# Optimization experiments

Hardware: AMD Instinct MI355X
Metric: run time of the kernel (lower is better)

Reference implementation:

```python
import jax, jax.numpy as jnp
import numpy as np

H = 16  # num_attention_heads


def setup_inputs() -> dict:
    key = jax.random.key(0)
    ks = jax.random.split(key, 4)
    B, S, D = 2, 2048, 1024
    hidden_states = jax.random.normal(ks[0], (B, S, D), dtype=jnp.float32)
    attention_mask = jnp.zeros((B, 1, 1, S), dtype=jnp.float32)
    scale = 1.0 / np.sqrt(D)
    Wq = jax.random.normal(ks[1], (D, D), dtype=jnp.float32) * scale
    Wk = jax.random.normal(ks[2], (D, D), dtype=jnp.float32) * scale
    Wv = jax.random.normal(ks[3], (D, D), dtype=jnp.float32) * scale
    bq = jnp.zeros((D,), dtype=jnp.float32)
    bk = jnp.zeros((D,), dtype=jnp.float32)
    bv = jnp.zeros((D,), dtype=jnp.float32)
    return {"hidden_states": hidden_states, "attention_mask": attention_mask,
            "Wq": Wq, "bq": bq, "Wk": Wk, "bk": bk, "Wv": Wv, "bv": bv}


def reference(hidden_states, attention_mask, Wq, bq, Wk, bk, Wv, bv):
    B, S, D = hidden_states.shape
    Dh = D // H

    def proj(W, b):
        # torch Linear: x @ W.T + b ; reshape to [B, H, S, Dh]
        y = jnp.einsum('bsd,ed->bse', hidden_states, W) + b
        return y.reshape(B, S, H, Dh).transpose(0, 2, 1, 3)

    q = proj(Wq, bq)
    k = proj(Wk, bk)
    v = proj(Wv, bv)

    scores = jnp.einsum('bhqd,bhkd->bhqk', q, k) / jnp.sqrt(jnp.float32(Dh))
    scores = scores + attention_mask  # additive mask broadcast [B,1,1,S]
    probs = jax.nn.softmax(scores, axis=-1)  # [B,H,Sq,Sk]
    out_attention_scores = probs.sum(axis=-2).sum(axis=-2)  # [B, Sk]
    # dropout prob = 0 (eval) -> identity
    context = jnp.einsum('bhqk,bhkd->bhqd', probs, v)
    context = context.transpose(0, 2, 1, 3).reshape(B, S, D)
    return context, out_attention_scores
```

## Files before the change

### kernel.cpp

```cpp
#include <hip/hip_runtime.h>
#include <hip/hip_bf16.h>
#include <stdint.h>

typedef unsigned short u16;
typedef __attribute__((ext_vector_type(8))) unsigned short u16x8;
typedef __attribute__((ext_vector_type(4))) unsigned short u16x4;
typedef __attribute__((ext_vector_type(8))) __bf16 bf16x8;
typedef __attribute__((ext_vector_type(4))) float f32x4;
typedef __attribute__((ext_vector_type(16))) float f32x16;

#define LOG2E 1.44269504088896340736f

#if defined(__has_builtin)
#if __has_builtin(__builtin_amdgcn_exp2f)
#define EXP2(x) __builtin_amdgcn_exp2f(x)
#endif
#endif
#ifndef EXP2
#define EXP2(x) exp2f(x)
#endif

__device__ __forceinline__ f32x4 mfma16(u16x8 a, u16x8 b, f32x4 c) {
  return __builtin_amdgcn_mfma_f32_16x16x32_bf16(
      __builtin_bit_cast(bf16x8, a), __builtin_bit_cast(bf16x8, b), c, 0, 0, 0);
}

__device__ __forceinline__ f32x16 mfma32(u16x8 a, u16x8 b, f32x16 c) {
  return __builtin_amdgcn_mfma_f32_32x32x16_bf16(
      __builtin_bit_cast(bf16x8, a), __builtin_bit_cast(bf16x8, b), c, 0, 0, 0);
}

__device__ __forceinline__ u16 f2bf(float f) {
  unsigned u = __builtin_bit_cast(unsigned, f);
  return (u16)((u + 0x7fffu + ((u >> 16) & 1u)) >> 16);
}

__device__ __forceinline__ unsigned cvtpk(float a, float b) {
  unsigned r;
  asm volatile("v_cvt_pk_bf16_f32 %0, %1, %2" : "=v"(r) : "v"(a), "v"(b));
  return r;
}

__device__ __forceinline__ void pswap(unsigned& a, unsigned& b) {
  asm volatile("v_permlane32_swap_b32 %0, %1" : "+v"(a), "+v"(b));
}

__device__ __forceinline__ void gload_lds16(const void* g, void* l) {
  __builtin_amdgcn_global_load_lds(
      (__attribute__((address_space(1))) void*)const_cast<void*>(g),
      (__attribute__((address_space(3))) void*)l, 16, 0, 0);
}

template<int N> __device__ __forceinline__ void vmwait() {
  asm volatile("s_waitcnt vmcnt(%0)" :: "n"(N) : "memory");
  __builtin_amdgcn_sched_barrier(0);
}

#define SWZ(row, colbyte) ((((row) * 128) + (colbyte)) ^ (((row) & 7) << 4))

__global__ void cast_f32_bf16(const float* __restrict__ src, u16* __restrict__ dst, int n4) {
  int i = blockIdx.x * blockDim.x + threadIdx.x;
  if (i < n4) {
    f32x4 v = ((const f32x4*)src)[i];
    u16x4 o;
    o[0] = f2bf(v[0]); o[1] = f2bf(v[1]); o[2] = f2bf(v[2]); o[3] = f2bf(v[3]);
    ((u16x4*)dst)[i] = o;
  }
}

__global__ void cast3_f32_bf16(const float* __restrict__ s0, const float* __restrict__ s1,
                               const float* __restrict__ s2, u16* __restrict__ dst) {
  const int seg = blockIdx.x >> 10;
  const int i = (blockIdx.x & 1023) * blockDim.x + threadIdx.x;
  const float* src = (seg == 0) ? s0 : ((seg == 1) ? s1 : s2);
  f32x4 v = ((const f32x4*)src)[i];
  u16x4 o;
  o[0] = f2bf(v[0]); o[1] = f2bf(v[1]); o[2] = f2bf(v[2]); o[3] = f2bf(v[3]);
  ((u16x4*)(dst + (size_t)seg * 1048576))[i] = o;
}

__global__ __launch_bounds__(256) void gemm_qkv(
    const u16* __restrict__ A, const u16* __restrict__ Bm,
    const float* __restrict__ bq, const float* __restrict__ bk, const float* __restrict__ bv,
    u16* __restrict__ Qb, u16* __restrict__ Kb, u16* __restrict__ VTb) {
  __shared__ __align__(16) u16 Asm[3][4096];
  __shared__ __align__(16) u16 Bsm[3][4096];
  const int tid = threadIdx.x;
  const int wave = tid >> 6, lane = tid & 63;
  const int lq = lane & 15, lg = lane >> 4;
  const int wr = wave >> 1, wc = wave & 1;
  const int lin = blockIdx.y * 24 + blockIdx.x;
  const int wg = (lin & 7) * 96 + (lin >> 3);
  const int m0 = (wg / 24) * 128, n0 = (wg % 24) * 128;

  f32x4 zero = {0.f, 0.f, 0.f, 0.f};
  f32x4 acc[4][4];
#pragma unroll
  for (int mi = 0; mi < 4; ++mi)
#pragma unroll
    for (int ni = 0; ni < 4; ++ni) acc[mi][ni] = zero;

  auto stage = [&](int kt, int buf) {
    const int k0 = kt * 32;
#pragma unroll
    for (int c = 0; c < 2; ++c) {
      const int idx = wave * 2 + c;
      const u16* ga = A + (size_t)(m0 + idx * 16 + (lane >> 2)) * 1024 + k0 + (lane & 3) * 8;
      gload_lds16(ga, (char*)&Asm[buf][0] + idx * 1024);
      const u16* gb = Bm + (size_t)(n0 + idx * 16 + (lane >> 2)) * 1024 + k0 + (lane & 3) * 8;
      gload_lds16(gb, (char*)&Bsm[buf][0] + idx * 1024);
    }
  };

  stage(0, 0);
  stage(1, 1);
  for (int kt = 0; kt < 32; ++kt) {
    if (kt < 31) vmwait<4>(); else vmwait<0>();
    __builtin_amdgcn_s_barrier();
    if (kt + 2 < 32) stage(kt + 2, (kt + 2) % 3);
    const int cur = kt % 3;

    __builtin_amdgcn_s_setprio(1);
    u16x8 af[4], bfr[4];
#pragma unroll
    for (int mi = 0; mi < 4; ++mi)
      af[mi] = *(const u16x8*)&Asm[cur][(wr * 64 + mi * 16 + lq) * 32 + lg * 8];
#pragma unroll
    for (int ni = 0; ni < 4; ++ni)
      bfr[ni] = *(const u16x8*)&Bsm[cur][(wc * 64 + ni * 16 + lq) * 32 + lg * 8];
#pragma unroll
    for (int mi = 0; mi < 4; ++mi)
#pragma unroll
      for (int ni = 0; ni < 4; ++ni)
        acc[mi][ni] = mfma16(af[mi], bfr[ni], acc[mi][ni]);
    __builtin_amdgcn_s_setprio(0);
  }

  const int which = n0 >> 10;
  const float* bias = (which == 0) ? bq : ((which == 1) ? bk : bv);
  const float scl = (which == 0) ? (0.125f * LOG2E) : 1.0f;
#pragma unroll
  for (int mi = 0; mi < 4; ++mi) {
    const int m = m0 + wr * 64 + mi * 16 + lg * 4;
    const int bb = m >> 11;
    const int s = m & 2047;
#pragma unroll
    for (int ni = 0; ni < 4; ++ni) {
      const int n = n0 + wc * 64 + ni * 16 + lq;
      const int d = n & 1023;
      const int h = d >> 6, dh = d & 63;
      const float bi = bias[d];
#pragma unroll
      for (int r = 0; r < 4; ++r) {
        float v = (acc[mi][ni][r] + bi) * scl;
        if (which == 2)
          VTb[(((size_t)bb * 16 + h) * 64 + dh) * 2048 + (size_t)(s + r)] = f2bf(v);
        else {
          u16* dst = (which == 0) ? Qb : Kb;
          dst[(((size_t)bb * 16 + h) * 2048 + (size_t)(s + r)) * 64 + dh] = f2bf(v);
        }
      }
    }
  }
}

__global__ __launch_bounds__(512) void attn_main(
    const u16* __restrict__ Qb, const u16* __restrict__ Kb, const u16* __restrict__ VTb,
    const float* __restrict__ maskg, float* __restrict__ out_ctx, float* __restrict__ winv) {
  __shared__ __align__(16) u16 Kl[3][4096];
  __shared__ __align__(16) u16 VTl[3][4096];
  __shared__ float sml[256];

  const int tid = threadIdx.x;
  const int w = tid >> 6, lane = tid & 63;
  const int l31 = lane & 31, h = lane >> 5;
  const int bid = (blockIdx.x & 7) * 32 + (blockIdx.x >> 3);
  const int qt = bid & 7, bh = bid >> 3;
  const int b = bh >> 4, hh = bh & 15;
  const int qw = qt * 256 + w * 32;

  const u16* qp = Qb + ((size_t)bh * 2048 + qw + l31) * 64 + h * 8;
  u16x8 qa[4];
#pragma unroll
  for (int dq = 0; dq < 4; ++dq) qa[dq] = *(const u16x8*)(qp + dq * 16);

  const char* Kbase = (const char*)(Kb + (size_t)bh * 2048 * 64);
  const char* VTbase = (const char*)(VTb + (size_t)bh * 64 * 2048);
  const float* mbase = maskg + b * 2048;

  const int srow = tid >> 3;
  const int scol = ((tid & 7) * 16) ^ ((srow & 7) << 4);
  auto stageK = [&](int kt, int buf) {
    gload_lds16(Kbase + (size_t)(kt * 64 + srow) * 128 + scol, (char*)&Kl[buf][0] + w * 1024);
  };
  auto stageVT = [&](int kt, int buf) {
    gload_lds16(VTbase + (size_t)srow * 4096 + (size_t)kt * 128 + scol, (char*)&VTl[buf][0] + w * 1024);
  };

  f32x16 accpv[2];
#pragma unroll
  for (int db = 0; db < 2; ++db)
#pragma unroll
    for (int r = 0; r < 16; ++r) accpv[db][r] = 0.f;
  float l_l = 0.f;

  stageK(0, 0); stageVT(0, 0);
  stageK(1, 1); stageVT(1, 1);
  for (int kt = 0; kt < 32; ++kt) {
    if (kt < 31) vmwait<2>(); else vmwait<0>();
    __builtin_amdgcn_s_barrier();
    const char* Kt = (const char*)&Kl[kt % 3][0];
    const char* Vt = (const char*)&VTl[kt % 3][0];

    __builtin_amdgcn_s_setprio(1);
#pragma unroll
    for (int kb = 0; kb < 2; ++kb) {
      f32x16 s;
#pragma unroll
      for (int r = 0; r < 16; ++r) s[r] = 0.f;
#pragma unroll
      for (int dq = 0; dq < 4; ++dq) {
        const u16x8 ka = *(const u16x8*)(Kt + SWZ(kb * 32 + l31, dq * 32 + h * 16));
        s = mfma32(ka, qa[dq], s);
      }
      float p[16];
#pragma unroll
      for (int g = 0; g < 4; ++g) {
        const f32x4 mv = *(const f32x4*)(mbase + kt * 64 + kb * 32 + g * 8 + h * 4);
#pragma unroll
        for (int j = 0; j < 4; ++j)
          p[g * 4 + j] = EXP2(fmaf(mv[j], LOG2E, s[g * 4 + j]));
      }
      l_l += ((p[0] + p[1]) + (p[2] + p[3])) + ((p[4] + p[5]) + (p[6] + p[7])) +
             ((p[8] + p[9]) + (p[10] + p[11])) + ((p[12] + p[13]) + (p[14] + p[15]));
      unsigned a01 = cvtpk(p[0], p[1]), a23 = cvtpk(p[2], p[3]);
      unsigned a45 = cvtpk(p[4], p[5]), a67 = cvtpk(p[6], p[7]);
      unsigned b01 = cvtpk(p[8], p[9]), b23 = cvtpk(p[10], p[11]);
      unsigned b45 = cvtpk(p[12], p[13]), b67 = cvtpk(p[14], p[15]);
      pswap(a01, a45); pswap(a23, a67);
      pswap(b01, b45); pswap(b23, b67);
      uint4 f1 = {a01, a23, a45, a67};
      uint4 f2 = {b01, b23, b45, b67};
      u16x8 pf[2] = {__builtin_bit_cast(u16x8, f1), __builtin_bit_cast(u16x8, f2)};
#pragma unroll
      for (int ks2 = 0; ks2 < 2; ++ks2) {
#pragma unroll
        for (int db = 0; db < 2; ++db) {
          const u16x8 vt = *(const u16x8*)(Vt + SWZ(db * 32 + l31, kb * 64 + ks2 * 32 + h * 16));
          accpv[db] = mfma32(pf[ks2], vt, accpv[db]);
        }
      }
    }
    __builtin_amdgcn_s_setprio(0);
    __builtin_amdgcn_sched_barrier(0);
    if (kt + 2 < 32) {
      stageK(kt + 2, (kt + 2) % 3);
      stageVT(kt + 2, (kt + 2) % 3);
    }
  }

  l_l += __shfl_xor(l_l, 32);
  const float il = 1.0f / l_l;
  if (h == 0) {
    winv[bh * 2048 + qw + l31] = il;
    sml[w * 32 + l31] = il;
  }
  __syncthreads();
  f32x4 il4[4];
#pragma unroll
  for (int g = 0; g < 4; ++g) il4[g] = *(const f32x4*)&sml[w * 32 + g * 8 + h * 4];

#pragma unroll
  for (int db = 0; db < 2; ++db) {
#pragma unroll
    for (int r = 0; r < 16; ++r) {
      const int q = qw + (r & 3) + (r >> 2) * 8 + h * 4;
      out_ctx[(size_t)(b * 2048 + q) * 1024 + hh * 64 + db * 32 + l31] =
          accpv[db][r] * il4[r >> 2][r & 3];
    }
  }
}

__global__ __launch_bounds__(256) void colsum_kernel(
    const u16* __restrict__ Qb, const u16* __restrict__ Kb,
    const float* __restrict__ maskg, const float* __restrict__ winv,
    float* __restrict__ out_cs) {
  __shared__ __align__(16) u16 Ql[3][4096];

  const int tid = threadIdx.x;
  const int w = tid >> 6, lane = tid & 63;
  const int lq = lane & 15, lg = lane >> 4;
  const int bid = (blockIdx.x & 7) * 64 + (blockIdx.x >> 3);
  const int ktile = bid & 15, bh = bid >> 4;
  const int b = bh >> 4;
  const int kbase = ktile * 128 + w * 32;

  const u16* kp0 = Kb + ((size_t)bh * 2048 + kbase + lq) * 64 + lg * 8;
  const u16* kp1 = kp0 + 16 * 64;
  const u16x8 kb00 = *(const u16x8*)kp0, kb01 = *(const u16x8*)(kp0 + 32);
  const u16x8 kb10 = *(const u16x8*)kp1, kb11 = *(const u16x8*)(kp1 + 32);
  const float mvl0 = maskg[b * 2048 + kbase + lq] * LOG2E;
  const float mvl1 = maskg[b * 2048 + kbase + 16 + lq] * LOG2E;
  const float* wbase = winv + bh * 2048;
  const char* Qbase = (const char*)(Qb + (size_t)bh * 2048 * 64);

  const int r0 = tid >> 3;
  const int scol = ((tid & 7) * 16) ^ ((r0 & 7) << 4);
  auto stageQ = [&](int qt, int buf) {
    const char* src = Qbase + (size_t)(qt * 64) * 128;
    char* d = (char*)&Ql[buf][0] + w * 1024;
    gload_lds16(src + (size_t)r0 * 128 + scol, d);
    gload_lds16(src + (size_t)(r0 + 32) * 128 + scol, d + 4096);
  };

  float c0 = 0.f, c1 = 0.f;
  stageQ(0, 0);
  stageQ(1, 1);
  for (int qt = 0; qt < 32; ++qt) {
    if (qt < 31) vmwait<2>(); else vmwait<0>();
    __builtin_amdgcn_s_barrier();
    const char* Qt = (const char*)&Ql[qt % 3][0];
    __builtin_amdgcn_s_setprio(1);
#pragma unroll
    for (int chunk = 0; chunk < 4; ++chunk) {
      const u16x8 qf0 = *(const u16x8*)(Qt + SWZ(chunk * 16 + lq, lg * 16));
      const u16x8 qf1 = *(const u16x8*)(Qt + SWZ(chunk * 16 + lq, 64 + lg * 16));
      f32x4 z = {0.f, 0.f, 0.f, 0.f};
      f32x4 s0 = mfma16(qf0, kb00, z);
      s0 = mfma16(qf1, kb01, s0);
      f32x4 s1 = mfma16(qf0, kb10, z);
      s1 = mfma16(qf1, kb11, s1);
      const f32x4 wv = *(const f32x4*)(wbase + qt * 64 + chunk * 16 + lg * 4);
#pragma unroll
      for (int r = 0; r < 4; ++r) {
        c0 += EXP2(s0[r] + mvl0) * wv[r];
        c1 += EXP2(s1[r] + mvl1) * wv[r];
      }
    }
    __builtin_amdgcn_s_setprio(0);
    __builtin_amdgcn_sched_barrier(0);
    if (qt + 2 < 32) stageQ(qt + 2, (qt + 2) % 3);
  }
  c0 += __shfl_xor(c0, 16); c0 += __shfl_xor(c0, 32);
  c1 += __shfl_xor(c1, 16); c1 += __shfl_xor(c1, 32);
  if (lg == 0) {
    atomicAdd(&out_cs[b * 2048 + kbase + lq], c0);
    atomicAdd(&out_cs[b * 2048 + kbase + 16 + lq], c1);
  }
}

extern "C" void kernel_launch(void* const* d_in, const int* in_sizes, int n_in,
                              void* d_out, int out_size, void* d_ws, size_t ws_size,
                              hipStream_t stream) {
  (void)in_sizes; (void)n_in; (void)out_size; (void)ws_size;
  const float* X    = (const float*)d_in[0];
  const float* mask = (const float*)d_in[1];
  const float* Wq   = (const float*)d_in[2];
  const float* bq   = (const float*)d_in[3];
  const float* Wk   = (const float*)d_in[4];
  const float* bk   = (const float*)d_in[5];
  const float* Wv   = (const float*)d_in[6];
  const float* bv   = (const float*)d_in[7];
  float* out = (float*)d_out;

  char* ws = (char*)d_ws;
  u16* Xb   = (u16*)(ws);
  u16* Wcat = (u16*)(ws + 8388608);
  u16* Qb   = (u16*)(ws + 14680064);
  u16* Kb   = (u16*)(ws + 23068672);
  u16* VTb  = (u16*)(ws + 31457280);
  float* winv = (float*)(ws + 39845888);

  cast_f32_bf16<<<4096, 256, 0, stream>>>(X, Xb, 1048576);
  cast3_f32_bf16<<<3072, 256, 0, stream>>>(Wq, Wk, Wv, Wcat);

  hipMemsetAsync(out + 4194304, 0, 4096 * sizeof(float), stream);

  gemm_qkv<<<dim3(24, 32), 256, 0, stream>>>(Xb, Wcat, bq, bk, bv, Qb, Kb, VTb);

  attn_main<<<256, 512, 0, stream>>>(Qb, Kb, VTb, mask, out, winv);
  colsum_kernel<<<512, 256, 0, stream>>>(Qb, Kb, mask, winv, out + 4194304);
}
```

Measured before the change: 155.7 us.

## Split attention and colsum over key/query halves with atomic accumulation

Splits the attention kernel's key range into two halves, doubling the grid to 512 blocks. Each block atomically adds its unnormalized context and row sums into zeroed buffers. A new normalize_ctx kernel then divides the context by the row sum and writes the inverse sums. The colsum kernel is likewise split over query halves to 1024 blocks. This aims to fill more compute units on a 256-CU part, at the cost of float atomics on the 16 MB context, an extra memset and an extra read/write pass over the context.

```diff
diff --git a/kernel.cpp b/kernel.cpp
--- a/kernel.cpp
+++ b/kernel.cpp
@@ -52,6 +52,7 @@
 }
 
 template<int N> __device__ __forceinline__ void vmwait() {
+  __builtin_amdgcn_sched_barrier(0);
   asm volatile("s_waitcnt vmcnt(%0)" :: "n"(N) : "memory");
   __builtin_amdgcn_sched_barrier(0);
 }
@@ -164,20 +165,20 @@
   }
 }
 
-__global__ __launch_bounds__(512) void attn_main(
+__global__ __launch_bounds__(512) void attn_split(
     const u16* __restrict__ Qb, const u16* __restrict__ Kb, const u16* __restrict__ VTb,
-    const float* __restrict__ maskg, float* __restrict__ out_ctx, float* __restrict__ winv) {
+    const float* __restrict__ maskg, float* __restrict__ out_ctx, float* __restrict__ pl) {
   __shared__ __align__(16) u16 Kl[3][4096];
   __shared__ __align__(16) u16 VTl[3][4096];
-  __shared__ float sml[256];
 
   const int tid = threadIdx.x;
   const int w = tid >> 6, lane = tid & 63;
   const int l31 = lane & 31, h = lane >> 5;
-  const int bid = (blockIdx.x & 7) * 32 + (blockIdx.x >> 3);
-  const int qt = bid & 7, bh = bid >> 3;
+  const int bid = (blockIdx.x & 7) * 64 + (blockIdx.x >> 3);
+  const int qt = bid & 7, kh = (bid >> 3) & 1, bh = bid >> 4;
   const int b = bh >> 4, hh = bh & 15;
   const int qw = qt * 256 + w * 32;
+  const int kt0 = kh * 16;
 
   const u16* qp = Qb + ((size_t)bh * 2048 + qw + l31) * 64 + h * 8;
   u16x8 qa[4];
@@ -204,13 +205,14 @@
     for (int r = 0; r < 16; ++r) accpv[db][r] = 0.f;
   float l_l = 0.f;
 
-  stageK(0, 0); stageVT(0, 0);
-  stageK(1, 1); stageVT(1, 1);
-  for (int kt = 0; kt < 32; ++kt) {
-    if (kt < 31) vmwait<2>(); else vmwait<0>();
+  stageK(kt0, 0); stageVT(kt0, 0);
+  stageK(kt0 + 1, 1); stageVT(kt0 + 1, 1);
+  for (int j = 0; j < 16; ++j) {
+    const int kt = kt0 + j;
+    if (j < 15) vmwait<2>(); else vmwait<0>();
     __builtin_amdgcn_s_barrier();
-    const char* Kt = (const char*)&Kl[kt % 3][0];
-    const char* Vt = (const char*)&VTl[kt % 3][0];
+    const char* Kt = (const char*)&Kl[j % 3][0];
+    const char* Vt = (const char*)&VTl[j % 3][0];
 
     __builtin_amdgcn_s_setprio(1);
 #pragma unroll
@@ -228,8 +230,8 @@
       for (int g = 0; g < 4; ++g) {
         const f32x4 mv = *(const f32x4*)(mbase + kt * 64 + kb * 32 + g * 8 + h * 4);
 #pragma unroll
-        for (int j = 0; j < 4; ++j)
-          p[g * 4 + j] = EXP2(fmaf(mv[j], LOG2E, s[g * 4 + j]));
+        for (int j2 = 0; j2 < 4; ++j2)
+          p[g * 4 + j2] = EXP2(fmaf(mv[j2], LOG2E, s[g * 4 + j2]));
       }
       l_l += ((p[0] + p[1]) + (p[2] + p[3])) + ((p[4] + p[5]) + (p[6] + p[7])) +
              ((p[8] + p[9]) + (p[10] + p[11])) + ((p[12] + p[13]) + (p[14] + p[15]));
@@ -253,32 +255,37 @@
     }
     __builtin_amdgcn_s_setprio(0);
     __builtin_amdgcn_sched_barrier(0);
-    if (kt + 2 < 32) {
-      stageK(kt + 2, (kt + 2) % 3);
-      stageVT(kt + 2, (kt + 2) % 3);
+    if (j + 2 < 16) {
+      stageK(kt0 + j + 2, (j + 2) % 3);
+      stageVT(kt0 + j + 2, (j + 2) % 3);
     }
   }
 
   l_l += __shfl_xor(l_l, 32);
-  const float il = 1.0f / l_l;
-  if (h == 0) {
-    winv[bh * 2048 + qw + l31] = il;
-    sml[w * 32 + l31] = il;
-  }
-  __syncthreads();
-  f32x4 il4[4];
-#pragma unroll
-  for (int g = 0; g < 4; ++g) il4[g] = *(const f32x4*)&sml[w * 32 + g * 8 + h * 4];
+  if (h == 0) atomicAdd(&pl[bh * 2048 + qw + l31], l_l);
 
 #pragma unroll
   for (int db = 0; db < 2; ++db) {
 #pragma unroll
     for (int r = 0; r < 16; ++r) {
       const int q = qw + (r & 3) + (r >> 2) * 8 + h * 4;
-      out_ctx[(size_t)(b * 2048 + q) * 1024 + hh * 64 + db * 32 + l31] =
-          accpv[db][r] * il4[r >> 2][r & 3];
-    }
-  }
+      atomicAdd(&out_ctx[(size_t)(b * 2048 + q) * 1024 + hh * 64 + db * 32 + l31],
+                accpv[db][r]);
+    }
+  }
+}
+
+__global__ __launch_bounds__(256) void normalize_ctx(
+    float* __restrict__ ctx, const float* __restrict__ pl, float* __restrict__ winv) {
+  const int idx = blockIdx.x * 256 + threadIdx.x;
+  const int row = idx >> 8;
+  const int c4 = idx & 255;
+  const int b = row >> 11, q = row & 2047, h = c4 >> 4;
+  const float il = 1.0f / pl[(b * 16 + h) * 2048 + q];
+  f32x4 v = ((const f32x4*)ctx)[idx];
+  v[0] *= il; v[1] *= il; v[2] *= il; v[3] *= il;
+  ((f32x4*)ctx)[idx] = v;
+  if ((c4 & 15) == 0) winv[(b * 16 + h) * 2048 + q] = il;
 }
 
 __global__ __launch_bounds__(256) void colsum_kernel(
@@ -290,10 +297,11 @@
   const int tid = threadIdx.x;
   const int w = tid >> 6, lane = tid & 63;
   const int lq = lane & 15, lg = lane >> 4;
-  const int bid = (blockIdx.x & 7) * 64 + (blockIdx.x >> 3);
-  const int ktile = bid & 15, bh = bid >> 4;
+  const int bid = (blockIdx.x & 7) * 128 + (blockIdx.x >> 3);
+  const int ktile = bid & 15, qh = (bid >> 4) & 1, bh = bid >> 5;
   const int b = bh >> 4;
   const int kbase = ktile * 128 + w * 32;
+  const int q0t = qh * 16;
 
   const u16* kp0 = Kb + ((size_t)bh * 2048 + kbase + lq) * 64 + lg * 8;
   const u16* kp1 = kp0 + 16 * 64;
@@ -314,12 +322,13 @@
   };
 
   float c0 = 0.f, c1 = 0.f;
-  stageQ(0, 0);
-  stageQ(1, 1);
-  for (int qt = 0; qt < 32; ++qt) {
-    if (qt < 31) vmwait<2>(); else vmwait<0>();
+  stageQ(q0t, 0);
+  stageQ(q0t + 1, 1);
+  for (int j = 0; j < 16; ++j) {
+    const int qt = q0t + j;
+    if (j < 15) vmwait<2>(); else vmwait<0>();
     __builtin_amdgcn_s_barrier();
-    const char* Qt = (const char*)&Ql[qt % 3][0];
+    const char* Qt = (const char*)&Ql[j % 3][0];
     __builtin_amdgcn_s_setprio(1);
 #pragma unroll
     for (int chunk = 0; chunk < 4; ++chunk) {
@@ -339,7 +348,7 @@
     }
     __builtin_amdgcn_s_setprio(0);
     __builtin_amdgcn_sched_barrier(0);
-    if (qt + 2 < 32) stageQ(qt + 2, (qt + 2) % 3);
+    if (j + 2 < 16) stageQ(q0t + j + 2, (j + 2) % 3);
   }
   c0 += __shfl_xor(c0, 16); c0 += __shfl_xor(c0, 32);
   c1 += __shfl_xor(c1, 16); c1 += __shfl_xor(c1, 32);
@@ -369,15 +378,18 @@
   u16* Qb   = (u16*)(ws + 14680064);
   u16* Kb   = (u16*)(ws + 23068672);
   u16* VTb  = (u16*)(ws + 31457280);
-  float* winv = (float*)(ws + 39845888);
+  float* pl   = (float*)(ws + 39845888);
+  float* winv = (float*)(ws + 40108032);
+
+  hipMemsetAsync(out, 0, (4194304 + 4096) * sizeof(float), stream);
+  hipMemsetAsync(pl, 0, 65536 * sizeof(float), stream);
 
   cast_f32_bf16<<<4096, 256, 0, stream>>>(X, Xb, 1048576);
   cast3_f32_bf16<<<3072, 256, 0, stream>>>(Wq, Wk, Wv, Wcat);
 
-  hipMemsetAsync(out + 4194304, 0, 4096 * sizeof(float), stream);
-
   gemm_qkv<<<dim3(24, 32), 256, 0, stream>>>(Xb, Wcat, bq, bk, bv, Qb, Kb, VTb);
 
-  attn_main<<<256, 512, 0, stream>>>(Qb, Kb, VTb, mask, out, winv);
-  colsum_kernel<<<512, 256, 0, stream>>>(Qb, Kb, mask, winv, out + 4194304);
-}
+  attn_split<<<512, 512, 0, stream>>>(Qb, Kb, VTb, mask, out, pl);
+  normalize_ctx<<<4096, 256, 0, stream>>>(out, pl, winv);
+  colsum_kernel<<<1024, 256, 0, stream>>>(Qb, Kb, mask, winv, out + 4194304);
+}
```

Result: slower. 169.7 us (+9.0%).
